# Performance work log

Measured on AMD Instinct MI355X. Metric: run time of the kernel, lower is better.

Reference implementation:

```python
import jax, jax.numpy as jnp
import numpy as np

NUM_GROUPS = 32
EPS = 1e-5


def group_norm(x, scale, bias):
    b, c, h, w = x.shape
    g = NUM_GROUPS
    xg = x.reshape(b, g, c // g, h, w)
    mean = xg.mean(axis=(2, 3, 4), keepdims=True)
    var = xg.var(axis=(2, 3, 4), keepdims=True)
    xn = (xg - mean) * jax.lax.rsqrt(var + EPS)
    xn = xn.reshape(b, c, h, w)
    return xn * scale[None, :, None, None] + bias[None, :, None, None]


def conv1x1(x, w, b):
    # x: [b,c,h,w], w: [o,c], b: [o]
    return jnp.einsum('oc,bchw->bohw', w, x) + b[None, :, None, None]


def setup_inputs() -> dict:
    key = jax.random.key(0)
    ks = jax.random.split(key, 8)
    b, c, h, w = 16, 512, 32, 32
    fan = 1.0 / np.sqrt(c)
    return {
        'x': jax.random.normal(ks[0], (b, c, h, w), dtype=jnp.float32),
        'time_emb': jax.random.normal(ks[1], (b, c), dtype=jnp.float32),
        'y': jax.random.randint(ks[2], (b,), 0, 1000, dtype=jnp.int64),
        'gn_scale': jnp.ones((c,), dtype=jnp.float32),
        'gn_bias': jnp.zeros((c,), dtype=jnp.float32),
        'w_qkv': jax.random.normal(ks[3], (3 * c, c), dtype=jnp.float32) * fan,
        'b_qkv': jax.random.normal(ks[4], (3 * c,), dtype=jnp.float32) * fan,
        'w_out': jax.random.normal(ks[5], (c, c), dtype=jnp.float32) * fan,
        'b_out': jax.random.normal(ks[6], (c,), dtype=jnp.float32) * fan,
    }


def reference(x, time_emb, y, gn_scale, gn_bias, w_qkv, b_qkv, w_out, b_out):
    b, c, h, w = x.shape
    qkv = conv1x1(group_norm(x, gn_scale, gn_bias), w_qkv, b_qkv)  # [b,3c,h,w]
    q, k, v = jnp.split(qkv, 3, axis=1)
    n = h * w
    q = q.transpose(0, 2, 3, 1).reshape(b, n, c)  # [b,n,c]
    k = k.reshape(b, c, n)                        # [b,c,n]
    v = v.transpose(0, 2, 3, 1).reshape(b, n, c)  # [b,n,c]
    scores = jnp.einsum('bnc,bcm->bnm', q, k) * (c ** -0.5)  # [b,n,n]
    attn = jax.nn.softmax(scores, axis=-1)
    out = jnp.einsum('bnm,bmc->bnc', attn, v)     # [b,n,c]
    out = out.reshape(b, h, w, c).transpose(0, 3, 1, 2)
    return conv1x1(out, w_out, b_out) + x
```

## Files before the change

kernel.cpp:

```cpp
#include <hip/hip_runtime.h>
#include <hip/hip_bf16.h>

#define NB   16
#define NC   512
#define NSPA 1024
#define GN_EPS 1e-5f
#define SCL 0.044194173824159216f

typedef __bf16 bf16x8 __attribute__((ext_vector_type(8)));
typedef __bf16 bf16x4 __attribute__((ext_vector_type(4)));
typedef float  f32x4  __attribute__((ext_vector_type(4)));

typedef __attribute__((address_space(3))) void lds_t;
typedef const __attribute__((address_space(1))) void gl_t;
#define GLDS16(g, l) __builtin_amdgcn_global_load_lds((gl_t*)(g), (lds_t*)(l), 16, 0, 0)

__device__ __forceinline__ __bf16 tob(float f) { return (__bf16)f; }

__device__ __forceinline__ int xcd_swz(int cpx) {
  return (blockIdx.x & 7) * cpx + (blockIdx.x >> 3);
}

__global__ void stats_w_kernel(const float* __restrict__ x,
                               const float* __restrict__ gn_scale,
                               const float* __restrict__ gn_bias,
                               const float* __restrict__ wq,
                               const float* __restrict__ wo,
                               const float* __restrict__ bqkv,
                               float* __restrict__ coefA, float* __restrict__ coefB,
                               __bf16* __restrict__ wqT, __bf16* __restrict__ wkT,
                               __bf16* __restrict__ wvT, __bf16* __restrict__ wob,
                               float* __restrict__ rvec, float* __restrict__ bc,
                               float* __restrict__ rowsum) {
  __shared__ __align__(16) unsigned char smem[9216];
  const int id = blockIdx.x;
  const int t = threadIdx.x;
  if (id < 512) {
    const int L = (id & 7) * 64 + (id >> 3);
    const int b = L >> 5, g = L & 31;
    const float4* base = (const float4*)(x + (size_t)(b * NC + g * 16) * NSPA);
    float s = 0.f, ss = 0.f;
#pragma unroll
    for (int i = 0; i < 16; ++i) {
      float4 v = base[i * 256 + t];
      s  += (v.x + v.y) + (v.z + v.w);
      ss += (v.x * v.x + v.y * v.y) + (v.z * v.z + v.w * v.w);
    }
#pragma unroll
    for (int off = 32; off; off >>= 1) {
      s  += __shfl_xor(s, off);
      ss += __shfl_xor(ss, off);
    }
    float* red = (float*)smem;
    const int wave = t >> 6, lane = t & 63;
    if (lane == 0) { red[wave] = s; red[4 + wave] = ss; }
    __syncthreads();
    if (t < 16) {
      const float S  = red[0] + red[1] + red[2] + red[3];
      const float SS = red[4] + red[5] + red[6] + red[7];
      const float mean = S * (1.f / 16384.f);
      const float var  = SS * (1.f / 16384.f) - mean * mean;
      const float rstd = rsqrtf(var + GN_EPS);
      const int c = g * 16 + t;
      const float a = gn_scale[c] * rstd;
      coefA[b * NC + c] = a;
      coefB[b * NC + c] = gn_bias[c] - mean * a;
    }
  } else if (id < 704) {
    const int id2 = id - 512;
    const int mat = id2 >> 6, tile = id2 & 63;
    const int o0 = (tile >> 3) * 64, c0 = (tile & 7) * 64;
    __bf16* dstT = (mat == 0) ? wqT : (mat == 1) ? wkT : wvT;
    __bf16 (*l)[72] = (__bf16(*)[72])smem;
    const int orr = t >> 2, seg = (t & 3) * 16;
    const float4* src = (const float4*)(wq + (size_t)(mat * NC + o0 + orr) * NC + c0 + seg);
#pragma unroll
    for (int i = 0; i < 4; ++i) {
      float4 v = src[i];
      l[seg + i * 4 + 0][orr] = tob(v.x);
      l[seg + i * 4 + 1][orr] = tob(v.y);
      l[seg + i * 4 + 2][orr] = tob(v.z);
      l[seg + i * 4 + 3][orr] = tob(v.w);
    }
    __syncthreads();
#pragma unroll
    for (int i = 0; i < 2; ++i) {
      const int chunk = t + i * 256;
      const int row = chunk >> 3, sg = chunk & 7;
      *(bf16x8*)(dstT + (size_t)(c0 + row) * NC + o0 + sg * 8) = *(const bf16x8*)&l[row][sg * 8];
    }
  } else if (id < 768) {
    const int idx = id - 704;
#pragma unroll
    for (int i = 0; i < 4; ++i) {
      const int tt = idx * 1024 + i * 256 + t;
      float4 v = ((const float4*)wo)[tt];
      bf16x4 w;
      w[0] = tob(v.x); w[1] = tob(v.y); w[2] = tob(v.z); w[3] = tob(v.w);
      *(bf16x4*)(wob + (size_t)tt * 4) = w;
    }
  } else if (id < 776) {
    const int c0 = (id - 768) * 64;
    const int lane = t & 63, wave = t >> 6;
    const int c = c0 + lane;
    float s = 0.f;
    for (int o = wave * 128; o < wave * 128 + 128; ++o)
      s += wq[(size_t)(NC + o) * NC + c] * bqkv[o];
    float* red = (float*)smem;
    red[wave * 64 + lane] = s;
    __syncthreads();
    if (wave == 0) {
      float tot = red[lane] + red[64 + lane] + red[128 + lane] + red[192 + lane];
      rvec[c] = tot;
    }
  } else if (id < 784) {
    const int o = (id - 776) * 64 + (t >> 2);
    const int q = t & 3;
    const float4* wr = (const float4*)(wo + (size_t)o * NC + q * 128);
    const float4* bv = (const float4*)(bqkv + 2 * NC + q * 128);
    float s = 0.f;
#pragma unroll
    for (int i = 0; i < 32; ++i) {
      float4 w4 = wr[i], b4 = bv[i];
      s += (w4.x * b4.x + w4.y * b4.y) + (w4.z * b4.z + w4.w * b4.w);
    }
    s += __shfl_xor(s, 1);
    s += __shfl_xor(s, 2);
    if (q == 0) bc[o] = s;
  } else {
    float4* dst = (float4*)(rowsum + (id - 784) * 4096);
#pragma unroll
    for (int i = 0; i < 4; ++i) dst[i * 256 + t] = make_float4(0.f, 0.f, 0.f, 0.f);
  }
}

__global__ void pack_x_kernel(const float* __restrict__ x,
                              const float* __restrict__ coefA,
                              const float* __restrict__ coefB,
                              __bf16* __restrict__ xnT) {
  const int L = xcd_swz(256);
  const int b = L >> 7, rem = L & 127;
  const int c0 = (rem >> 4) * 64, n0 = (rem & 15) * 64;
  __shared__ __bf16 l[64][72];
  const int tid = threadIdx.x;
  const int cl = tid >> 2, seg = (tid & 3) * 16;
  const float ca = coefA[b * NC + c0 + cl], cb = coefB[b * NC + c0 + cl];
  const float4* src = (const float4*)(x + (size_t)(b * NC + c0 + cl) * NSPA + n0 + seg);
#pragma unroll
  for (int i = 0; i < 4; ++i) {
    float4 v = src[i];
    l[seg + i * 4 + 0][cl] = tob(v.x * ca + cb);
    l[seg + i * 4 + 1][cl] = tob(v.y * ca + cb);
    l[seg + i * 4 + 2][cl] = tob(v.z * ca + cb);
    l[seg + i * 4 + 3][cl] = tob(v.w * ca + cb);
  }
  __syncthreads();
#pragma unroll
  for (int i = 0; i < 2; ++i) {
    const int chunk = tid + i * 256;
    const int row = chunk >> 3, s = chunk & 7;
    *(bf16x8*)(xnT + (size_t)(b * NSPA + n0 + row) * NC + c0 + s * 8) =
        *(const bf16x8*)&l[row][s * 8];
  }
}

template <int MROWS>
__device__ __forceinline__ void stage_pair(const __bf16* __restrict__ A, int lda,
                                           const __bf16* __restrict__ B, int ldb,
                                           int k0, __bf16* lAf, __bf16* lBf) {
  const int tid = threadIdx.x;
#pragma unroll
  for (int i = 0; i < 4; ++i) {
    const int idx = tid + i * 256;
    const int srow = idx >> 3;
    const int ss = ((idx & 7) ^ (srow & 7)) * 8;
    GLDS16(B + (size_t)srow * ldb + k0 + ss, lBf + idx * 8);
  }
#pragma unroll
  for (int i = 0; i < MROWS / 32; ++i) {
    const int idx = tid + i * 256;
    const int srow = idx >> 3;
    const int ss = ((idx & 7) ^ (srow & 7)) * 8;
    GLDS16(A + (size_t)srow * lda + k0 + ss, lAf + idx * 8);
  }
}

template <int MROWS>
__device__ __forceinline__ void gemm_core_sb(const __bf16* __restrict__ A, int lda,
                                             const __bf16* __restrict__ B, int ldb,
                                             int K, __bf16 (*lA)[64],
                                             __bf16 (*lB)[64], f32x4 (*acc)[4]) {
  constexpr int MH = MROWS / 32;
  const int tid = threadIdx.x;
  const int lane = tid & 63, wave = tid >> 6;
  const int wm = (wave >> 1) * (MROWS / 2), wn = (wave & 1) * 64;
  const int fr = lane & 15, fg = (lane >> 4) * 8;
  const int nt = K >> 6;

  for (int t = 0; t < nt; ++t) {
    stage_pair<MROWS>(A, lda, B, ldb, t * 64, &lA[0][0], &lB[0][0]);
    __syncthreads();
    __builtin_amdgcn_s_setprio(1);
#pragma unroll
    for (int ks = 0; ks < 2; ++ks) {
      bf16x8 af[MH], bfr[4];
#pragma unroll
      for (int mi = 0; mi < MH; ++mi) {
        const int r = wm + mi * 16 + fr;
        af[mi] = *(const bf16x8*)&lA[r][(ks * 32 + fg) ^ ((r & 7) << 3)];
      }
#pragma unroll
      for (int ni = 0; ni < 4; ++ni) {
        const int r = wn + ni * 16 + fr;
        bfr[ni] = *(const bf16x8*)&lB[r][(ks * 32 + fg) ^ ((r & 7) << 3)];
      }
#pragma unroll
      for (int mi = 0; mi < MH; ++mi)
#pragma unroll
        for (int ni = 0; ni < 4; ++ni)
          acc[mi][ni] = __builtin_amdgcn_mfma_f32_16x16x32_bf16(af[mi], bfr[ni], acc[mi][ni], 0, 0, 0);
    }
    __builtin_amdgcn_s_setprio(0);
    if (t + 1 < nt) __syncthreads();
  }
}

__global__ __launch_bounds__(256, 4) void mid_kernel(
    const __bf16* __restrict__ wqT, const __bf16* __restrict__ wkT,
    const __bf16* __restrict__ wvT, const __bf16* __restrict__ wob,
    const __bf16* __restrict__ xnT, const float* __restrict__ rvec,
    __bf16* __restrict__ Aproj, float* __restrict__ R) {
  __shared__ __bf16 lA[128][64], lB[128][64];
  const int id = blockIdx.x;
  if (id < 32) {
    const bool doM = id < 16;
    const int sub = doM ? id : id - 16;
    const int mt = sub >> 2, nt2 = sub & 3;
    const __bf16* A = doM ? (wqT + (size_t)mt * 128 * NC) : (wob + (size_t)mt * 128 * NC);
    const __bf16* B = doM ? (wkT + (size_t)nt2 * 128 * NC) : (wvT + (size_t)nt2 * 128 * NC);
    f32x4 acc[4][4] = {};
    gemm_core_sb<128>(A, NC, B, NC, NC, lA, lB, acc);

    const int tid = threadIdx.x;
    const int lane = tid & 63, wave = tid >> 6;
    const int wm = (wave >> 1) * 64, wn = (wave & 1) * 64;
    const int fr = lane & 15, fq4 = (lane >> 4) * 4;
    const int mbase = (doM ? 0 : NC) + mt * 128;
#pragma unroll
    for (int mi = 0; mi < 4; ++mi) {
      const int m = mbase + wm + mi * 16 + fq4;
#pragma unroll
      for (int ni = 0; ni < 4; ++ni) {
        const int n = nt2 * 128 + wn + ni * 16 + fr;
#pragma unroll
        for (int r = 0; r < 4; ++r)
          Aproj[(size_t)(m + r) * NC + n] = tob(acc[mi][ni][r]);
      }
    }
  } else {
    const int id2 = id - 32;
    const int L = (id2 & 7) * 32 + (id2 >> 3);
    const int b = L >> 4, j0 = (L & 15) * 64;
    const int row = threadIdx.x >> 2, q = threadIdx.x & 3;
    const __bf16* src = xnT + ((size_t)(b * NSPA) + j0 + row) * NC + q * 128;
    const float* rv = rvec + q * 128;
    float s = 0.f;
#pragma unroll
    for (int i = 0; i < 16; ++i) {
      bf16x8 v = *(const bf16x8*)(src + i * 8);
#pragma unroll
      for (int e = 0; e < 8; ++e) s += (float)v[e] * rv[i * 8 + e];
    }
    s += __shfl_xor(s, 1);
    s += __shfl_xor(s, 2);
    if (q == 0) R[b * NSPA + j0 + row] = s;
  }
}

__global__ __launch_bounds__(256, 4) void proj_kernel(
    const __bf16* __restrict__ Aproj, const __bf16* __restrict__ xnT,
    const float* __restrict__ bc, __bf16* __restrict__ Yt, __bf16* __restrict__ vp) {
  const int L = xcd_swz(128);
  const int pair = L >> 3, mblk = L & 7;
  const int b = pair >> 3;
  const int n0 = (pair & 7) * 128, m0 = mblk * 128;
  __shared__ __bf16 lA[128][64], lB[128][64];
  f32x4 acc[4][4] = {};
  gemm_core_sb<128>(Aproj + (size_t)m0 * NC, NC, xnT + ((size_t)b * NSPA + n0) * NC, NC,
                    NC, lA, lB, acc);

  const int lane = threadIdx.x & 63, wave = threadIdx.x >> 6;
  const int wm = (wave >> 1) * 64, wn = (wave & 1) * 64;
  const int fr = lane & 15, fq4 = (lane >> 4) * 4;
  if (m0 < NC) {
#pragma unroll
    for (int mi = 0; mi < 4; ++mi) {
      const int m = m0 + wm + mi * 16 + fq4;
#pragma unroll
      for (int ni = 0; ni < 4; ++ni) {
        const int n = n0 + wn + ni * 16 + fr;
        bf16x4 w;
        w[0] = tob(acc[mi][ni][0]);
        w[1] = tob(acc[mi][ni][1]);
        w[2] = tob(acc[mi][ni][2]);
        w[3] = tob(acc[mi][ni][3]);
        *(bf16x4*)(Yt + ((size_t)b * NSPA + n) * NC + m) = w;
      }
    }
  } else {
#pragma unroll
    for (int mi = 0; mi < 4; ++mi) {
      const int m = m0 + wm + mi * 16 + fq4;
      const int d = m - NC;
      const float4 bias = *(const float4*)(bc + d);
#pragma unroll
      for (int ni = 0; ni < 4; ++ni) {
        const int n = n0 + wn + ni * 16 + fr;
        vp[((size_t)b * NC + d + 0) * NSPA + n] = tob(acc[mi][ni][0] + bias.x);
        vp[((size_t)b * NC + d + 1) * NSPA + n] = tob(acc[mi][ni][1] + bias.y);
        vp[((size_t)b * NC + d + 2) * NSPA + n] = tob(acc[mi][ni][2] + bias.z);
        vp[((size_t)b * NC + d + 3) * NSPA + n] = tob(acc[mi][ni][3] + bias.w);
      }
    }
  }
}

__global__ __launch_bounds__(256, 4) void scores_kernel(
    const __bf16* __restrict__ Yt, const __bf16* __restrict__ xnT,
    const float* __restrict__ R, __bf16* __restrict__ P,
    float* __restrict__ rowsum) {
  const int L = xcd_swz(128);
  const int b = L >> 6, r = L & 63;
  const int i0 = (r >> 3) * 128, j0 = (r & 7) * 128;
  __shared__ __bf16 lA[128][64], lB[128][64];
  f32x4 acc[4][4] = {};
  gemm_core_sb<128>(Yt + ((size_t)b * NSPA + j0) * NC, NC,
                    xnT + ((size_t)b * NSPA + i0) * NC, NC, NC, lA, lB, acc);

  const int lane = threadIdx.x & 63, wave = threadIdx.x >> 6;
  const int wm = (wave >> 1) * 64, wn = (wave & 1) * 64;
  const int fr = lane & 15, fq4 = (lane >> 4) * 4;
  float rsum[4] = {0.f, 0.f, 0.f, 0.f};
#pragma unroll
  for (int mi = 0; mi < 4; ++mi) {
    const int j = j0 + wm + mi * 16 + fq4;
    const float4 Rb = *(const float4*)(R + b * NSPA + j);
#pragma unroll
    for (int ni = 0; ni < 4; ++ni) {
      const int i = i0 + wn + ni * 16 + fr;
      bf16x4 w;
      w[0] = tob(__expf((acc[mi][ni][0] + Rb.x) * SCL));
      w[1] = tob(__expf((acc[mi][ni][1] + Rb.y) * SCL));
      w[2] = tob(__expf((acc[mi][ni][2] + Rb.z) * SCL));
      w[3] = tob(__expf((acc[mi][ni][3] + Rb.w) * SCL));
      rsum[ni] += ((float)w[0] + (float)w[1]) + ((float)w[2] + (float)w[3]);
      *(bf16x4*)(P + ((size_t)b * NSPA + i) * NSPA + j) = w;
    }
  }
#pragma unroll
  for (int ni = 0; ni < 4; ++ni) {
    rsum[ni] += __shfl_xor(rsum[ni], 16);
    rsum[ni] += __shfl_xor(rsum[ni], 32);
  }
  if (lane < 16) {
#pragma unroll
    for (int ni = 0; ni < 4; ++ni)
      atomicAdd(&rowsum[b * NSPA + i0 + wn + ni * 16 + fr], rsum[ni]);
  }
}

__global__ __launch_bounds__(256, 4) void pvout_kernel(
    const __bf16* __restrict__ vp, const __bf16* __restrict__ P,
    const float* __restrict__ rowsum, const float* __restrict__ bout,
    const float* __restrict__ x, float* __restrict__ out) {
  const int L = xcd_swz(128);
  const int b = L >> 6, r = L & 63;
  const int d0 = (r >> 3) * 64, i0 = (r & 7) * 128;
  __shared__ __bf16 lA[64][64], lB[128][64];
  f32x4 acc[2][4] = {};
  gemm_core_sb<64>(vp + ((size_t)b * NC + d0) * NSPA, NSPA,
                   P + ((size_t)b * NSPA + i0) * NSPA, NSPA, NSPA, lA, lB, acc);

  const int lane = threadIdx.x & 63, wave = threadIdx.x >> 6;
  const int wm = (wave >> 1) * 32, wn = (wave & 1) * 64;
  const int fr = lane & 15, fq4 = (lane >> 4) * 4;
  float inv[4];
#pragma unroll
  for (int ni = 0; ni < 4; ++ni)
    inv[ni] = 1.f / rowsum[b * NSPA + i0 + wn + ni * 16 + fr];
#pragma unroll
  for (int mi = 0; mi < 2; ++mi) {
    const int d = d0 + wm + mi * 16 + fq4;
    const float4 bias = *(const float4*)(bout + d);
#pragma unroll
    for (int ni = 0; ni < 4; ++ni) {
      const int i = i0 + wn + ni * 16 + fr;
      const size_t ix = ((size_t)b * NC + d) * NSPA + i;
      out[ix + 0 * NSPA] = acc[mi][ni][0] * inv[ni] + bias.x + x[ix + 0 * NSPA];
      out[ix + 1 * NSPA] = acc[mi][ni][1] * inv[ni] + bias.y + x[ix + 1 * NSPA];
      out[ix + 2 * NSPA] = acc[mi][ni][2] * inv[ni] + bias.z + x[ix + 2 * NSPA];
      out[ix + 3 * NSPA] = acc[mi][ni][3] * inv[ni] + bias.w + x[ix + 3 * NSPA];
    }
  }
}

extern "C" void kernel_launch(void* const* d_in, const int* in_sizes, int n_in,
                              void* d_out, int out_size, void* d_ws, size_t ws_size,
                              hipStream_t stream) {
  const float* x        = (const float*)d_in[0];
  const float* gn_scale = (const float*)d_in[3];
  const float* gn_bias  = (const float*)d_in[4];
  const float* w_qkv    = (const float*)d_in[5];
  const float* b_qkv    = (const float*)d_in[6];
  const float* w_out    = (const float*)d_in[7];
  const float* b_out    = (const float*)d_in[8];
  float* out = (float*)d_out;

  float*  coefA  = (float*)d_ws;
  float*  coefB  = coefA + NB * NC;
  float*  rvec   = coefB + NB * NC;
  float*  bc     = rvec + NC;
  float*  R      = bc + NC;
  float*  rowsum = R + NB * NSPA;
  __bf16* wqT    = (__bf16*)(rowsum + NB * NSPA);
  __bf16* wkT    = wqT + NC * NC;
  __bf16* wvT    = wkT + NC * NC;
  __bf16* wob    = wvT + NC * NC;
  __bf16* Aproj  = wob + NC * NC;
  __bf16* xnT    = Aproj + 2 * NC * NC;
  __bf16* vp     = xnT + (size_t)NB * NSPA * NC;
  __bf16* P      = vp + (size_t)NB * NC * NSPA;
  __bf16* Yt     = (__bf16*)d_out;

  stats_w_kernel<<<dim3(788), 256, 0, stream>>>(x, gn_scale, gn_bias, w_qkv, w_out,
                                                b_qkv, coefA, coefB, wqT, wkT, wvT,
                                                wob, rvec, bc, rowsum);
  pack_x_kernel<<<dim3(2048), 256, 0, stream>>>(x, coefA, coefB, xnT);
  mid_kernel<<<dim3(288), 256, 0, stream>>>(wqT, wkT, wvT, wob, xnT, rvec, Aproj, R);
  proj_kernel<<<dim3(1024), 256, 0, stream>>>(Aproj, xnT, bc, Yt, vp);
  scores_kernel<<<dim3(1024), 256, 0, stream>>>(Yt, xnT, R, P, rowsum);
  pvout_kernel<<<dim3(1024), 256, 0, stream>>>(vp, P, rowsum, b_out, x, out);
}
```

Baseline: 119.8 us.

## Fuse x packing with weight-product GEMM and compute R from LDS tile

Merges the pack_x kernel and the mid kernel into one launch. The packing blocks now also compute the R dot-product from the normalized tile already in LDS, accumulating into R with atomics, so xnT no longer has to be re-read from global memory. R is zeroed in the stats kernel. This removes one kernel launch and one pass over xnT, at the cost of atomics on R and a shared-memory footprint set by the larger GEMM branch.

Measured after the change: 117.3 us. 1.02x faster.

```diff
diff --git a/kernel.cpp b/kernel.cpp
--- a/kernel.cpp
+++ b/kernel.cpp
@@ -31,7 +31,7 @@
                                __bf16* __restrict__ wqT, __bf16* __restrict__ wkT,
                                __bf16* __restrict__ wvT, __bf16* __restrict__ wob,
                                float* __restrict__ rvec, float* __restrict__ bc,
-                               float* __restrict__ rowsum) {
+                               float* __restrict__ rowsum, float* __restrict__ R) {
   __shared__ __align__(16) unsigned char smem[9216];
   const int id = blockIdx.x;
   const int t = threadIdx.x;
@@ -128,39 +128,11 @@
     s += __shfl_xor(s, 2);
     if (q == 0) bc[o] = s;
   } else {
-    float4* dst = (float4*)(rowsum + (id - 784) * 4096);
+    const int z = id - 784;
+    float* tgt = (z < 4) ? (rowsum + z * 4096) : (R + (z - 4) * 4096);
+    float4* dst = (float4*)tgt;
 #pragma unroll
     for (int i = 0; i < 4; ++i) dst[i * 256 + t] = make_float4(0.f, 0.f, 0.f, 0.f);
-  }
-}
-
-__global__ void pack_x_kernel(const float* __restrict__ x,
-                              const float* __restrict__ coefA,
-                              const float* __restrict__ coefB,
-                              __bf16* __restrict__ xnT) {
-  const int L = xcd_swz(256);
-  const int b = L >> 7, rem = L & 127;
-  const int c0 = (rem >> 4) * 64, n0 = (rem & 15) * 64;
-  __shared__ __bf16 l[64][72];
-  const int tid = threadIdx.x;
-  const int cl = tid >> 2, seg = (tid & 3) * 16;
-  const float ca = coefA[b * NC + c0 + cl], cb = coefB[b * NC + c0 + cl];
-  const float4* src = (const float4*)(x + (size_t)(b * NC + c0 + cl) * NSPA + n0 + seg);
-#pragma unroll
-  for (int i = 0; i < 4; ++i) {
-    float4 v = src[i];
-    l[seg + i * 4 + 0][cl] = tob(v.x * ca + cb);
-    l[seg + i * 4 + 1][cl] = tob(v.y * ca + cb);
-    l[seg + i * 4 + 2][cl] = tob(v.z * ca + cb);
-    l[seg + i * 4 + 3][cl] = tob(v.w * ca + cb);
-  }
-  __syncthreads();
-#pragma unroll
-  for (int i = 0; i < 2; ++i) {
-    const int chunk = tid + i * 256;
-    const int row = chunk >> 3, s = chunk & 7;
-    *(bf16x8*)(xnT + (size_t)(b * NSPA + n0 + row) * NC + c0 + s * 8) =
-        *(const bf16x8*)&l[row][s * 8];
   }
 }
 
@@ -225,23 +197,60 @@
   }
 }
 
-__global__ __launch_bounds__(256, 4) void mid_kernel(
+__global__ __launch_bounds__(256, 4) void pack_mid_kernel(
+    const float* __restrict__ x, const float* __restrict__ coefA,
+    const float* __restrict__ coefB, const float* __restrict__ rvec,
     const __bf16* __restrict__ wqT, const __bf16* __restrict__ wkT,
     const __bf16* __restrict__ wvT, const __bf16* __restrict__ wob,
-    const __bf16* __restrict__ xnT, const float* __restrict__ rvec,
-    __bf16* __restrict__ Aproj, float* __restrict__ R) {
-  __shared__ __bf16 lA[128][64], lB[128][64];
+    __bf16* __restrict__ xnT, float* __restrict__ R,
+    __bf16* __restrict__ Aproj) {
+  __shared__ __align__(16) __bf16 smem[2 * 128 * 64];
   const int id = blockIdx.x;
-  if (id < 32) {
-    const bool doM = id < 16;
-    const int sub = doM ? id : id - 16;
+  const int tid = threadIdx.x;
+  if (id < 2048) {
+    const int L = (id & 7) * 256 + (id >> 3);
+    const int b = L >> 7, rem = L & 127;
+    const int c0 = (rem >> 4) * 64, n0 = (rem & 15) * 64;
+    __bf16 (*l)[72] = (__bf16(*)[72])smem;
+    const int cl = tid >> 2, seg = (tid & 3) * 16;
+    const float ca = coefA[b * NC + c0 + cl], cb = coefB[b * NC + c0 + cl];
+    const float4* src = (const float4*)(x + (size_t)(b * NC + c0 + cl) * NSPA + n0 + seg);
+#pragma unroll
+    for (int i = 0; i < 4; ++i) {
+      float4 v = src[i];
+      l[seg + i * 4 + 0][cl] = tob(v.x * ca + cb);
+      l[seg + i * 4 + 1][cl] = tob(v.y * ca + cb);
+      l[seg + i * 4 + 2][cl] = tob(v.z * ca + cb);
+      l[seg + i * 4 + 3][cl] = tob(v.w * ca + cb);
+    }
+    __syncthreads();
+#pragma unroll
+    for (int i = 0; i < 2; ++i) {
+      const int chunk = tid + i * 256;
+      const int row = chunk >> 3, s = chunk & 7;
+      *(bf16x8*)(xnT + (size_t)(b * NSPA + n0 + row) * NC + c0 + s * 8) =
+          *(const bf16x8*)&l[row][s * 8];
+    }
+    const int nn = tid >> 2, q = tid & 3;
+    const float* rv = rvec + c0 + q * 16;
+    float s = 0.f;
+#pragma unroll
+    for (int i = 0; i < 16; ++i) s += (float)l[nn][q * 16 + i] * rv[i];
+    s += __shfl_xor(s, 1);
+    s += __shfl_xor(s, 2);
+    if (q == 0) atomicAdd(&R[b * NSPA + n0 + nn], s);
+  } else {
+    const int sub0 = id - 2048;
+    const bool doM = sub0 < 16;
+    const int sub = doM ? sub0 : sub0 - 16;
     const int mt = sub >> 2, nt2 = sub & 3;
     const __bf16* A = doM ? (wqT + (size_t)mt * 128 * NC) : (wob + (size_t)mt * 128 * NC);
     const __bf16* B = doM ? (wkT + (size_t)nt2 * 128 * NC) : (wvT + (size_t)nt2 * 128 * NC);
+    __bf16 (*lA)[64] = (__bf16(*)[64])smem;
+    __bf16 (*lB)[64] = (__bf16(*)[64])(smem + 128 * 64);
     f32x4 acc[4][4] = {};
     gemm_core_sb<128>(A, NC, B, NC, NC, lA, lB, acc);
 
-    const int tid = threadIdx.x;
     const int lane = tid & 63, wave = tid >> 6;
     const int wm = (wave >> 1) * 64, wn = (wave & 1) * 64;
     const int fr = lane & 15, fq4 = (lane >> 4) * 4;
@@ -257,23 +266,6 @@
           Aproj[(size_t)(m + r) * NC + n] = tob(acc[mi][ni][r]);
       }
     }
-  } else {
-    const int id2 = id - 32;
-    const int L = (id2 & 7) * 32 + (id2 >> 3);
-    const int b = L >> 4, j0 = (L & 15) * 64;
-    const int row = threadIdx.x >> 2, q = threadIdx.x & 3;
-    const __bf16* src = xnT + ((size_t)(b * NSPA) + j0 + row) * NC + q * 128;
-    const float* rv = rvec + q * 128;
-    float s = 0.f;
-#pragma unroll
-    for (int i = 0; i < 16; ++i) {
-      bf16x8 v = *(const bf16x8*)(src + i * 8);
-#pragma unroll
-      for (int e = 0; e < 8; ++e) s += (float)v[e] * rv[i * 8 + e];
-    }
-    s += __shfl_xor(s, 1);
-    s += __shfl_xor(s, 2);
-    if (q == 0) R[b * NSPA + j0 + row] = s;
   }
 }
 
@@ -432,11 +424,11 @@
   __bf16* P      = vp + (size_t)NB * NC * NSPA;
   __bf16* Yt     = (__bf16*)d_out;
 
-  stats_w_kernel<<<dim3(788), 256, 0, stream>>>(x, gn_scale, gn_bias, w_qkv, w_out,
+  stats_w_kernel<<<dim3(792), 256, 0, stream>>>(x, gn_scale, gn_bias, w_qkv, w_out,
                                                 b_qkv, coefA, coefB, wqT, wkT, wvT,
-                                                wob, rvec, bc, rowsum);
-  pack_x_kernel<<<dim3(2048), 256, 0, stream>>>(x, coefA, coefB, xnT);
-  mid_kernel<<<dim3(288), 256, 0, stream>>>(wqT, wkT, wvT, wob, xnT, rvec, Aproj, R);
+                                                wob, rvec, bc, rowsum, R);
+  pack_mid_kernel<<<dim3(2080), 256, 0, stream>>>(x, coefA, coefB, rvec, wqT, wkT,
+                                                  wvT, wob, xnT, R, Aproj);
   proj_kernel<<<dim3(1024), 256, 0, stream>>>(Aproj, xnT, bc, Yt, vp);
   scores_kernel<<<dim3(1024), 256, 0, stream>>>(Yt, xnT, R, P, rowsum);
   pvout_kernel<<<dim3(1024), 256, 0, stream>>>(vp, P, rowsum, b_out, x, out);
```
